# Kernel optimization log

Measured on AMD Instinct MI355X. Metric: run time of the kernel, lower is better.

Reference implementation:

```python
import jax, jax.numpy as jnp
import numpy as np

N_NODES = 100000
N_GRAPHS = 64
EPS = 1e-5


def _sage_conv(x, src, dst, Wl, bl, Wr):
    # mean-aggregate neighbor messages (src -> dst), then lin_l(agg) + lin_r(x)
    n = x.shape[0]
    deg = jax.ops.segment_sum(jnp.ones_like(dst, dtype=x.dtype), dst, num_segments=n)
    agg = jax.ops.segment_sum(x[src], dst, num_segments=n)  # [N, d]
    agg = agg / jnp.maximum(deg, 1.0)[:, None]
    return agg @ Wl + bl + x @ Wr


def _bn_relu(x, gamma, beta):
    mu = jnp.mean(x, axis=0)
    var = jnp.var(x, axis=0)
    return jax.nn.relu((x - mu) * jax.lax.rsqrt(var + EPS) * gamma + beta)


def setup_inputs() -> dict:
    key = jax.random.key(0)
    ks = jax.random.split(key, 16)
    E = 1600000
    x = jax.random.normal(ks[0], (N_NODES, 2), dtype=jnp.float32)
    edge_index = jax.random.randint(ks[1], (2, E), 0, N_NODES, dtype=jnp.int64)
    batch = jnp.sort(jax.random.randint(ks[2], (N_NODES,), 0, N_GRAPHS, dtype=jnp.int64))

    def lin(k, din, dout):
        s = 1.0 / np.sqrt(din)
        return jax.random.uniform(k, (din, dout), jnp.float32, -s, s)

    d = {"x": x, "edge_index": edge_index, "batch": batch}
    dims = [(2, 32), (32, 64), (64, 128)]
    for i, (din, dout) in enumerate(dims, 1):
        k1, k2 = jax.random.split(ks[2 + i])
        d[f"Wl{i}"] = lin(k1, din, dout)
        d[f"bl{i}"] = jnp.zeros((dout,), jnp.float32)
        d[f"Wr{i}"] = lin(k2, din, dout)
        d[f"g{i}"] = jnp.ones((dout,), jnp.float32)
        d[f"be{i}"] = jnp.zeros((dout,), jnp.float32)
    d["Wf1"] = lin(ks[10], 128, 64)
    d["bf1"] = jnp.zeros((64,), jnp.float32)
    d["Wf2"] = lin(ks[11], 64, 1)
    d["bf2"] = jnp.zeros((1,), jnp.float32)
    return d


def reference(x, edge_index, batch,
              Wl1, bl1, Wr1, g1, be1,
              Wl2, bl2, Wr2, g2, be2,
              Wl3, bl3, Wr3, g3, be3,
              Wf1, bf1, Wf2, bf2):
    src, dst = edge_index[0], edge_index[1]
    h = _bn_relu(_sage_conv(x, src, dst, Wl1, bl1, Wr1), g1, be1)
    h = _bn_relu(_sage_conv(h, src, dst, Wl2, bl2, Wr2), g2, be2)
    h = _bn_relu(_sage_conv(h, src, dst, Wl3, bl3, Wr3), g3, be3)
    # global mean pool over graphs
    cnt = jax.ops.segment_sum(jnp.ones_like(batch, dtype=h.dtype), batch, num_segments=N_GRAPHS)
    pooled = jax.ops.segment_sum(h, batch, num_segments=N_GRAPHS) / jnp.maximum(cnt, 1.0)[:, None]
    out = jax.nn.relu(pooled @ Wf1 + bf1)
    # dropout is identity in eval mode
    return out @ Wf2 + bf2
```

## Files before the change

kernel.cpp:

```cpp
#include <hip/hip_runtime.h>
#include <hip/hip_fp16.h>

#define N_NODES 100000
#define N_GRAPHS 64
#define BN_EPS 1e-5

#define NBF 391
#define PT1 4096
#define CAPF 4608

typedef _Float16 f16x8 __attribute__((ext_vector_type(8)));
typedef float f32x4 __attribute__((ext_vector_type(4)));

union F16x8u {
    f16x8 v;
    __half2 h2[4];
    uint4 u;
};

__device__ __forceinline__ float bfly64(float v) {
#pragma unroll
    for (int m = 1; m < 64; m <<= 1) v += __shfl_xor(v, m, 64);
    return v;
}

__device__ __forceinline__ unsigned pack_h2(float a, float b) {
    __half2 h = __floats2half2_rn(a, b);
    unsigned w;
    __builtin_memcpy(&w, &h, 4);
    return w;
}

__device__ __forceinline__ float2 unpack_h2(unsigned w) {
    __half2 h;
    __builtin_memcpy(&h, &w, 4);
    return __half22float2(h);
}

__global__ __launch_bounds__(256)
void pack_w(const float* __restrict__ Wl2, const float* __restrict__ Wr2,
            const float* __restrict__ Wl3, const float* __restrict__ Wr3,
            __half* __restrict__ pk, int* __restrict__ fcur,
            double* __restrict__ zero_region) {
    int tid = threadIdx.x;
    if (blockIdx.x == 0) {
        for (int t = tid; t < NBF; t += 256) fcur[t] = t * CAPF;
    } else if (blockIdx.x <= 4) {
        for (int i = (blockIdx.x - 1) * 256 + tid; i < 8960; i += 1024)
            zero_region[i] = 0.0;
    }
    int e = blockIdx.x * 256 + tid;
    const float* W; int le, DOUT, NCB, base, SZ;
    if (e < 2048)       { W = Wl2; le = e;         DOUT = 64;  NCB = 4; base = 0;     SZ = 2048; }
    else if (e < 4096)  { W = Wr2; le = e - 2048;  DOUT = 64;  NCB = 4; base = 4096;  SZ = 2048; }
    else if (e < 12288) { W = Wl3; le = e - 4096;  DOUT = 128; NCB = 8; base = 8192;  SZ = 8192; }
    else                { W = Wr3; le = e - 12288; DOUT = 128; NCB = 8; base = 24576; SZ = 8192; }
    int i = le & 7;
    int lane = (le >> 3) & 63;
    int cbkb = le >> 9;
    int cb = cbkb % NCB;
    int kb = cbkb / NCB;
    int k = kb * 32 + ((lane >> 4) << 3) + i;
    int col = cb * 16 + (lane & 15);
    float w = W[k * DOUT + col];
    __half h = __float2half(w);
    float lo = w - __half2float(h);
    pk[base + le] = h;
    pk[base + SZ + le] = __float2half(lo);
}


__global__ __launch_bounds__(256)
void part1(const int* __restrict__ dst, const int* __restrict__ src,
           int* __restrict__ fcur, int* __restrict__ qpk, int E) {
    __shared__ int ld[PT1];
    __shared__ unsigned short lb[PT1];
    __shared__ int hist[NBF], lbase[NBF], gbase[NBF];
    __shared__ int pairs[256];
    long long t0 = (long long)blockIdx.x * PT1;
    int n = (int)min((long long)PT1, (long long)E - t0);
    int tid = threadIdx.x;
    for (int i = tid; i < NBF; i += 256) hist[i] = 0;
    __syncthreads();
    int p[PT1 / 256], c[PT1 / 256];
#pragma unroll
    for (int k = 0; k < PT1 / 256; ++k) {
        int li = k * 256 + tid;
        if (li < n) {
            int d = __builtin_nontemporal_load(dst + t0 + li);
            int s = __builtin_nontemporal_load(src + t0 + li);
            c[k] = d >> 8;
            p[k] = ((d & 255) << 17) | s;
            atomicAdd(&hist[c[k]], 1);
        }
    }
    __syncthreads();
    int h0 = (2 * tid < NBF) ? hist[2 * tid] : 0;
    int h1 = (2 * tid + 1 < NBF) ? hist[2 * tid + 1] : 0;
    pairs[tid] = h0 + h1;
    __syncthreads();
    for (int st = 1; st < 256; st <<= 1) {
        int v = (tid >= st) ? pairs[tid - st] : 0;
        __syncthreads();
        pairs[tid] += v;
        __syncthreads();
    }
    int pe = tid ? pairs[tid - 1] : 0;
    if (2 * tid < NBF) lbase[2 * tid] = pe;
    if (2 * tid + 1 < NBF) lbase[2 * tid + 1] = pe + h0;
    __syncthreads();
    for (int b = tid; b < NBF; b += 256)
        gbase[b] = atomicAdd(&fcur[b], hist[b]);
    __syncthreads();
    for (int i = tid; i < NBF; i += 256) hist[i] = 0;
    __syncthreads();
#pragma unroll
    for (int k = 0; k < PT1 / 256; ++k) {
        int li = k * 256 + tid;
        if (li < n) {
            int pos = lbase[c[k]] + atomicAdd(&hist[c[k]], 1);
            ld[pos] = p[k]; lb[pos] = (unsigned short)c[k];
        }
    }
    __syncthreads();
    for (int i = tid; i < n; i += 256) {
        int bb = lb[i];
        int g = gbase[bb] + (i - lbase[bb]);
        qpk[g] = ld[i];
    }
}

__global__ __launch_bounds__(256)
void fill_final(const int* __restrict__ qpk, const int* __restrict__ fcur,
                int* __restrict__ offs, int* __restrict__ oend,
                int* __restrict__ nbr, int N) {
    __shared__ int cnt[256], cbase[256], cur[256];
    __shared__ int lout[CAPF];
    int b = blockIdx.x;
    int nlo = b << 8;
    int nn = min(256, N - nlo);
    int ebeg = b * CAPF;
    int ne = fcur[b] - ebeg;
    int tid = threadIdx.x;
    cnt[tid] = 0; cur[tid] = 0;
    __syncthreads();
    for (int i = tid; i < ne; i += 256)
        atomicAdd(&cnt[(qpk[ebeg + i] >> 17) & 255], 1);
    __syncthreads();
    cbase[tid] = cnt[tid];
    __syncthreads();
    for (int st = 1; st < 256; st <<= 1) {
        int v = (tid >= st) ? cbase[tid - st] : 0;
        __syncthreads();
        cbase[tid] += v;
        __syncthreads();
    }
    if (tid < nn) {
        offs[nlo + tid] = ebeg + (tid ? cbase[tid - 1] : 0);
        oend[nlo + tid] = ebeg + cbase[tid];
    }
    __syncthreads();
    for (int i = tid; i < ne; i += 256) {
        int p = qpk[ebeg + i];
        int ln = (p >> 17) & 255;
        int pos = (ln ? cbase[ln - 1] : 0) + atomicAdd(&cur[ln], 1);
        lout[pos] = p & 0x1FFFF;
    }
    __syncthreads();
    for (int i = tid; i < ne; i += 256)
        nbr[ebeg + i] = lout[i];
}

__global__ __launch_bounds__(256)
void layer1_fused(const float2* __restrict__ x2,
                  const int* __restrict__ offs, const int* __restrict__ oend,
                  const int* __restrict__ nbr,
                  const float* __restrict__ Wl, const float* __restrict__ bl,
                  const float* __restrict__ Wr,
                  __half* __restrict__ hout16,
                  double* __restrict__ sums, int N) {
    __shared__ float sAr[64];
    int tid = threadIdx.x;
    if (tid < 64) sAr[tid] = 0.f;
    __syncthreads();
    int n = blockIdx.x * 256 + tid;
    bool valid = (n < N);
    int beg = 0, end = 0;
    if (valid) { beg = offs[n]; end = oend[n]; }
    float ax0 = 0.f, ay0 = 0.f, ax1 = 0.f, ay1 = 0.f;
    int j = beg;
    for (; j + 16 <= end; j += 16) {
        int s[16];
#pragma unroll
        for (int u = 0; u < 16; ++u) s[u] = __builtin_nontemporal_load(nbr + j + u);
        float2 v[16];
#pragma unroll
        for (int u = 0; u < 16; ++u) v[u] = x2[s[u]];
#pragma unroll
        for (int u = 0; u < 16; ++u) {
            if (u & 1) { ax1 += v[u].x; ay1 += v[u].y; }
            else       { ax0 += v[u].x; ay0 += v[u].y; }
        }
    }
    for (; j + 4 <= end; j += 4) {
        int s[4];
#pragma unroll
        for (int u = 0; u < 4; ++u) s[u] = __builtin_nontemporal_load(nbr + j + u);
        float2 v[4];
#pragma unroll
        for (int u = 0; u < 4; ++u) v[u] = x2[s[u]];
        ax0 += v[0].x; ay0 += v[0].y;
        ax1 += v[1].x; ay1 += v[1].y;
        ax0 += v[2].x; ay0 += v[2].y;
        ax1 += v[3].x; ay1 += v[3].y;
    }
    for (; j < end; ++j) {
        float2 v = x2[nbr[j]];
        ax0 += v.x; ay0 += v.y;
    }
    float invd = 1.0f / fmaxf((float)(end - beg), 1.0f);
    float a0 = (ax0 + ax1) * invd, a1 = (ay0 + ay1) * invd;
    float x0 = 0.f, x1 = 0.f;
    if (valid) {
        float2 xv = x2[n];
        x0 = xv.x; x1 = xv.y;
    }
    float acc[32];
#pragma unroll
    for (int jj = 0; jj < 32; ++jj)
        acc[jj] = bl[jj] + a0 * Wl[jj] + a1 * Wl[32 + jj] + x0 * Wr[jj] + x1 * Wr[32 + jj];
    if (valid) {
        unsigned w[16];
#pragma unroll
        for (int p = 0; p < 16; ++p) w[p] = pack_h2(acc[2*p], acc[2*p+1]);
        uint4* q = (uint4*)(hout16 + (size_t)n * 32);
        q[0] = make_uint4(w[0], w[1], w[2], w[3]);
        q[1] = make_uint4(w[4], w[5], w[6], w[7]);
        q[2] = make_uint4(w[8], w[9], w[10], w[11]);
        q[3] = make_uint4(w[12], w[13], w[14], w[15]);
    }
    int lane = tid & 63;
#pragma unroll
    for (int jj = 0; jj < 32; ++jj) {
        float v = valid ? acc[jj] : 0.f;
        float s = bfly64(v);
        float q = bfly64(v * v);
        if (lane == jj) atomicAdd(&sAr[jj], s);
        if (lane == 32 + jj) atomicAdd(&sAr[32 + jj], q);
    }
    __syncthreads();
    if (tid < 64) atomicAdd(&sums[tid], (double)sAr[tid]);
}

template<int F>
__global__ __launch_bounds__(256)
void bn_apply(const uint4* __restrict__ h, const double* __restrict__ sums,
              const float* __restrict__ gamma, const float* __restrict__ beta,
              uint4* __restrict__ out, int N) {
    __shared__ __align__(16) float lsc[F], lsf[F];
    int tid = threadIdx.x;
    if (tid < F) {
        double mu = sums[tid] / (double)N_NODES;
        double var = sums[F + tid] / (double)N_NODES - mu * mu;
        if (var < 0.0) var = 0.0;
        double sc = (double)gamma[tid] / sqrt(var + BN_EPS);
        lsc[tid] = (float)sc;
        lsf[tid] = (float)((double)beta[tid] - mu * sc);
    }
    __syncthreads();
    constexpr int FV = F / 8;
    int total = N * FV;
    for (int i = blockIdx.x * 256 + tid; i < total; i += gridDim.x * 256) {
        uint4 v = h[i];
        int c4 = (i & (FV - 1)) * 2;
        float4 sca = ((const float4*)lsc)[c4];
        float4 scb = ((const float4*)lsc)[c4 + 1];
        float4 sfa = ((const float4*)lsf)[c4];
        float4 sfb = ((const float4*)lsf)[c4 + 1];
        float2 f0 = unpack_h2(v.x), f1 = unpack_h2(v.y);
        float2 f2 = unpack_h2(v.z), f3 = unpack_h2(v.w);
        uint4 o;
        o.x = pack_h2(fmaxf(f0.x * sca.x + sfa.x, 0.f), fmaxf(f0.y * sca.y + sfa.y, 0.f));
        o.y = pack_h2(fmaxf(f1.x * sca.z + sfa.z, 0.f), fmaxf(f1.y * sca.w + sfa.w, 0.f));
        o.z = pack_h2(fmaxf(f2.x * scb.x + sfb.x, 0.f), fmaxf(f2.y * scb.y + sfb.y, 0.f));
        o.w = pack_h2(fmaxf(f3.x * scb.z + sfb.z, 0.f), fmaxf(f3.y * scb.w + sfb.w, 0.f));
        out[i] = o;
    }
}

__device__ __forceinline__ void accum8_h16(float* acc, uint4 v) {
    float2 f0 = unpack_h2(v.x), f1 = unpack_h2(v.y);
    float2 f2 = unpack_h2(v.z), f3 = unpack_h2(v.w);
    acc[0] += f0.x; acc[1] += f0.y; acc[2] += f1.x; acc[3] += f1.y;
    acc[4] += f2.x; acc[5] += f2.y; acc[6] += f3.x; acc[7] += f3.y;
}

template<int F>
__global__ __launch_bounds__(256)
void agg_sum(const uint4* __restrict__ xb, const int* __restrict__ offs,
             const int* __restrict__ oend, const int* __restrict__ nbr,
             uint4* __restrict__ aggh, int N) {
    constexpr int FV = F / 8;
    constexpr int NPB = 256 / FV;
    int n = blockIdx.x * NPB + threadIdx.y;
    if (n >= N) return;
    int f = threadIdx.x;
    int beg = offs[n], end = oend[n];
    float a0[8], a1[8];
#pragma unroll
    for (int q = 0; q < 8; ++q) { a0[q] = 0.f; a1[q] = 0.f; }
    int j = beg;
    for (; j + 16 <= end; j += 16) {
        int s[16];
#pragma unroll
        for (int u = 0; u < 16; ++u) s[u] = __builtin_nontemporal_load(nbr + j + u);
        uint4 v[16];
#pragma unroll
        for (int u = 0; u < 16; ++u) v[u] = xb[s[u] * FV + f];
#pragma unroll
        for (int u = 0; u < 16; ++u)
            accum8_h16((u & 1) ? a1 : a0, v[u]);
    }
    if (j + 8 <= end) {
        int s[8];
#pragma unroll
        for (int u = 0; u < 8; ++u) s[u] = __builtin_nontemporal_load(nbr + j + u);
        uint4 v[8];
#pragma unroll
        for (int u = 0; u < 8; ++u) v[u] = xb[s[u] * FV + f];
#pragma unroll
        for (int u = 0; u < 8; ++u)
            accum8_h16((u & 1) ? a1 : a0, v[u]);
        j += 8;
    }
    if (j + 4 <= end) {
        int s[4];
#pragma unroll
        for (int u = 0; u < 4; ++u) s[u] = __builtin_nontemporal_load(nbr + j + u);
        uint4 v[4];
#pragma unroll
        for (int u = 0; u < 4; ++u) v[u] = xb[s[u] * FV + f];
#pragma unroll
        for (int u = 0; u < 4; ++u)
            accum8_h16((u & 1) ? a1 : a0, v[u]);
        j += 4;
    }
    for (; j < end; ++j) {
        uint4 v = xb[__builtin_nontemporal_load(nbr + j) * FV + f];
        accum8_h16(a0, v);
    }
    float invd = 1.0f / fmaxf((float)(end - beg), 1.0f);
    uint4 o;
    o.x = pack_h2((a0[0] + a1[0]) * invd, (a0[1] + a1[1]) * invd);
    o.y = pack_h2((a0[2] + a1[2]) * invd, (a0[3] + a1[3]) * invd);
    o.z = pack_h2((a0[4] + a1[4]) * invd, (a0[5] + a1[5]) * invd);
    o.w = pack_h2((a0[6] + a1[6]) * invd, (a0[7] + a1[7]) * invd);
    aggh[n * FV + f] = o;
}

template<int DIN, int DOUT>
__global__ __launch_bounds__(256)
void linear_mfma(const __half* __restrict__ bnx16, const __half* __restrict__ agg16,
                 const __half* __restrict__ wlhi, const __half* __restrict__ wllo,
                 const __half* __restrict__ wrhi, const __half* __restrict__ wrlo,
                 const float* __restrict__ bl,
                 __half* __restrict__ hout16, float* __restrict__ partial, int N) {
    constexpr int KB = DIN / 32;
    constexpr int NCB = DOUT / 16;
    constexpr int MREP = 2;
    constexpr int MB = 4 * MREP * 16;
    __shared__ float blkS[DOUT], blkQ[DOUT];
    int tid = threadIdx.x;
    for (int i = tid; i < DOUT; i += 256) { blkS[i] = 0.f; blkQ[i] = 0.f; }
    __syncthreads();
    int n0 = blockIdx.x * MB;

    int wave = tid >> 6;
    int lane = tid & 63;
    int rlane = lane & 15;
    int kg = lane >> 4;
    int rbase = n0 + wave * (MREP * 16);

    f16x8 aA[MREP][KB], aX[MREP][KB];
#pragma unroll
    for (int m = 0; m < MREP; ++m) {
        int row = rbase + m * 16 + rlane;
        int rowc = min(row, N - 1);
#pragma unroll
        for (int kb = 0; kb < KB; ++kb) {
            int c0 = kb * 32 + kg * 8;
            F16x8u ta, tx;
            ta.u = *(const uint4*)(agg16 + (size_t)rowc * DIN + c0);
            tx.u = *(const uint4*)(bnx16 + (size_t)rowc * DIN + c0);
            aA[m][kb] = ta.v;
            aX[m][kb] = tx.v;
        }
    }

    f32x4 acc[MREP][NCB];
#pragma unroll
    for (int cb = 0; cb < NCB; ++cb) {
        float bv = bl[cb * 16 + rlane];
#pragma unroll
        for (int m = 0; m < MREP; ++m)
            acc[m][cb] = {bv, bv, bv, bv};
    }

#pragma unroll
    for (int cb = 0; cb < NCB; ++cb) {
#pragma unroll
        for (int kb = 0; kb < KB; ++kb) {
            size_t fo = ((size_t)(kb * NCB + cb) * 64 + lane) * 8;
            f16x8 blh = *(const f16x8*)(wlhi + fo);
            f16x8 bll = *(const f16x8*)(wllo + fo);
            f16x8 brh = *(const f16x8*)(wrhi + fo);
            f16x8 brl = *(const f16x8*)(wrlo + fo);
#pragma unroll
            for (int m = 0; m < MREP; ++m) {
                acc[m][cb] = __builtin_amdgcn_mfma_f32_16x16x32_f16(aA[m][kb], blh, acc[m][cb], 0, 0, 0);
                acc[m][cb] = __builtin_amdgcn_mfma_f32_16x16x32_f16(aA[m][kb], bll, acc[m][cb], 0, 0, 0);
                acc[m][cb] = __builtin_amdgcn_mfma_f32_16x16x32_f16(aX[m][kb], brh, acc[m][cb], 0, 0, 0);
                acc[m][cb] = __builtin_amdgcn_mfma_f32_16x16x32_f16(aX[m][kb], brl, acc[m][cb], 0, 0, 0);
            }
        }
    }

#pragma unroll
    for (int m = 0; m < MREP; ++m) {
        int rowb = rbase + m * 16 + kg * 4;
#pragma unroll
        for (int r = 0; r < 4; ++r) {
            int node = rowb + r;
            if (node < N) {
#pragma unroll
                for (int cb = 0; cb < NCB; ++cb)
                    hout16[(size_t)node * DOUT + cb * 16 + rlane] = __float2half(acc[m][cb][r]);
            }
        }
    }

#pragma unroll
    for (int cb = 0; cb < NCB; ++cb) {
        float s = 0.f, q = 0.f;
#pragma unroll
        for (int m = 0; m < MREP; ++m) {
            int rowb = rbase + m * 16 + kg * 4;
#pragma unroll
            for (int r = 0; r < 4; ++r) {
                if (rowb + r < N) {
                    float v = acc[m][cb][r];
                    s += v; q += v * v;
                }
            }
        }
        s += __shfl_xor(s, 16, 64); s += __shfl_xor(s, 32, 64);
        q += __shfl_xor(q, 16, 64); q += __shfl_xor(q, 32, 64);
        if (kg == 0) {
            atomicAdd(&blkS[cb * 16 + rlane], s);
            atomicAdd(&blkQ[cb * 16 + rlane], q);
        }
    }
    __syncthreads();
    float* po = partial + (size_t)blockIdx.x * (2 * DOUT);
    for (int i = tid; i < DOUT; i += 256) {
        po[i] = blkS[i];
        po[DOUT + i] = blkQ[i];
    }
}

template<int F>
__global__ __launch_bounds__(256)
void stats_finalize2(const float* __restrict__ partial, double* __restrict__ sums, int P) {
    __shared__ double sh[256];
    int i = blockIdx.x;
    int t = threadIdx.x;
    double a = 0.0;
    for (int k = t; k < P; k += 256)
        a += (double)partial[(size_t)k * (2 * F) + i];
    sh[t] = a;
    __syncthreads();
    for (int st = 128; st > 0; st >>= 1) {
        if (t < st) sh[t] += sh[t + st];
        __syncthreads();
    }
    if (t == 0) sums[i] = sh[0];
}

__global__ void pool_partial(const __half* __restrict__ h, const int* __restrict__ batch,
                             const double* __restrict__ sums,
                             const float* __restrict__ gamma, const float* __restrict__ beta,
                             double* __restrict__ pooled_d, int N) {
    __shared__ float lsc[128], lsf[128];
    const int CH = 64;
    int f = threadIdx.x;
    {
        double mu = sums[f] / (double)N_NODES;
        double var = sums[128 + f] / (double)N_NODES - mu * mu;
        if (var < 0.0) var = 0.0;
        double sc = (double)gamma[f] / sqrt(var + BN_EPS);
        lsc[f] = (float)sc;
        lsf[f] = (float)((double)beta[f] - mu * sc);
    }
    __syncthreads();
    int n0 = blockIdx.x * CH;
    if (n0 >= N) return;
    int n1 = min(n0 + CH, N);
    float sc = lsc[f], sf = lsf[f];
    int g = batch[n0];
    float acc = 0.f;
    for (int n = n0; n < n1; ++n) {
        int bg = batch[n];
        if (bg != g) {
            atomicAdd(&pooled_d[g * 128 + f], (double)acc);
            acc = 0.f;
            g = bg;
        }
        float v = __half2float(h[(long long)n * 128 + f]);
        acc += fmaxf(v * sc + sf, 0.f);
    }
    atomicAdd(&pooled_d[g * 128 + f], (double)acc);
}

__global__ void mlp_fused(const double* __restrict__ pooled_d, const int* __restrict__ batch,
                          const float* __restrict__ Wf1, const float* __restrict__ bf1,
                          const float* __restrict__ Wf2, const float* __restrict__ bf2,
                          float* __restrict__ out, int N) {
    __shared__ float sp[128];
    int g = blockIdx.x;
    int t = threadIdx.x;
    int lo = 0, hi = N;
    while (lo < hi) { int m = (lo + hi) >> 1; if (batch[m] < g) lo = m + 1; else hi = m; }
    int start = lo;
    hi = N;
    while (lo < hi) { int m = (lo + hi) >> 1; if (batch[m] < g + 1) lo = m + 1; else hi = m; }
    int cnt = lo - start;
    sp[t] = (float)(pooled_d[g * 128 + t] / (double)max(cnt, 1));
    __syncthreads();
    if (t < 64) {
        float hacc = bf1[t];
#pragma unroll 8
        for (int k = 0; k < 128; ++k) hacc += sp[k] * Wf1[k * 64 + t];
        hacc = fmaxf(hacc, 0.f) * Wf2[t];
        for (int o = 32; o > 0; o >>= 1) hacc += __shfl_down(hacc, o);
        if (t == 0) out[g] = hacc + bf2[0];
    }
}

extern "C" void kernel_launch(void* const* d_in, const int* in_sizes, int n_in,
                              void* d_out, int out_size, void* d_ws, size_t ws_size,
                              hipStream_t stream) {
    const float* x     = (const float*)d_in[0];
    const int*   ei    = (const int*)d_in[1];
    const int*   batch = (const int*)d_in[2];
    const float *Wl1=(const float*)d_in[3],  *bl1=(const float*)d_in[4],  *Wr1=(const float*)d_in[5];
    const float *g1 =(const float*)d_in[6],  *be1=(const float*)d_in[7];
    const float *Wl2=(const float*)d_in[8],  *bl2=(const float*)d_in[9],  *Wr2=(const float*)d_in[10];
    const float *g2 =(const float*)d_in[11], *be2=(const float*)d_in[12];
    const float *Wl3=(const float*)d_in[13], *bl3=(const float*)d_in[14], *Wr3=(const float*)d_in[15];
    const float *g3 =(const float*)d_in[16], *be3=(const float*)d_in[17];
    const float *Wf1=(const float*)d_in[18], *bf1=(const float*)d_in[19];
    const float *Wf2=(const float*)d_in[20], *bf2=(const float*)d_in[21];

    const int N = N_NODES;
    const int E = in_sizes[1] / 2;
    const int* src = ei;
    const int* dst = ei + E;

    char* ws = (char*)d_ws;
    size_t off = 0;
    auto salloc = [&](size_t bytes) {
        void* p = ws + off;
        off += (bytes + 255) & ~(size_t)255;
        return p;
    };
    double* sums    = (double*)salloc(768 * 8);
    double* pooledd = (double*)salloc((size_t)N_GRAPHS * 128 * 8);
    int*    offs    = (int*)   salloc((size_t)N * 4);
    int*    oend    = (int*)   salloc((size_t)N * 4);
    int*    fcur    = (int*)   salloc((NBF + 1) * 4);
    int*    nbr     = (int*)   salloc((size_t)NBF * CAPF * 4);
    float*  partial = (float*) salloc((size_t)1024 * 256 * 4);
    __half* pk      = (__half*)salloc((size_t)40960 * 2);
    __half* h1h     = (__half*)salloc((size_t)(N + 256) * 32 * 2);
    __half* b1h     = (__half*)salloc((size_t)(N + 256) * 32 * 2);
    __half* h2h     = (__half*)salloc((size_t)(N + 256) * 64 * 2);
    __half* b2h     = (__half*)salloc((size_t)(N + 256) * 64 * 2);
    __half* h3h     = (__half*)salloc((size_t)(N + 256) * 128 * 2);
    __half* aggh    = (__half*)salloc((size_t)(N + 256) * 64 * 2);
    (void)ws_size;

    double* sums1 = sums, *sums2 = sums + 256, *sums3 = sums + 512;
    int* qpk = (int*)aggh;

    const __half *pwl2h = pk,         *pwl2l = pk + 2048;
    const __half *pwr2h = pk + 4096,  *pwr2l = pk + 6144;
    const __half *pwl3h = pk + 8192,  *pwl3l = pk + 16384;
    const __half *pwr3h = pk + 24576, *pwr3l = pk + 32768;

    pack_w<<<80, 256, 0, stream>>>(Wl2, Wr2, Wl3, Wr3, pk, fcur, sums);

    part1<<<(E + PT1 - 1) / PT1, 256, 0, stream>>>(dst, src, fcur, qpk, E);
    fill_final<<<NBF, 256, 0, stream>>>(qpk, fcur, offs, oend, nbr, N);

    const int NL = (N + 255) / 256;
    const int NBLK = (N + 127) / 128;

    layer1_fused<<<NL, 256, 0, stream>>>((const float2*)x, offs, oend, nbr,
                                          Wl1, bl1, Wr1, h1h, sums1, N);

    bn_apply<32><<<512, 256, 0, stream>>>((const uint4*)h1h, sums1, g1, be1, (uint4*)b1h, N);
    agg_sum<32><<<(N + 63) / 64, dim3(4, 64), 0, stream>>>(
        (const uint4*)b1h, offs, oend, nbr, (uint4*)aggh, N);
    linear_mfma<32, 64><<<NBLK, 256, 0, stream>>>(
        b1h, (const __half*)aggh, pwl2h, pwl2l, pwr2h, pwr2l, bl2, h2h, partial, N);
    stats_finalize2<64><<<128, 256, 0, stream>>>(partial, sums2, NBLK);

    bn_apply<64><<<512, 256, 0, stream>>>((const uint4*)h2h, sums2, g2, be2, (uint4*)b2h, N);
    agg_sum<64><<<(N + 31) / 32, dim3(8, 32), 0, stream>>>(
        (const uint4*)b2h, offs, oend, nbr, (uint4*)aggh, N);
    linear_mfma<64, 128><<<NBLK, 256, 0, stream>>>(
        b2h, (const __half*)aggh, pwl3h, pwl3l, pwr3h, pwr3l, bl3, h3h, partial, N);
    stats_finalize2<128><<<256, 256, 0, stream>>>(partial, sums3, NBLK);

    pool_partial<<<(N + 63) / 64, 128, 0, stream>>>(h3h, batch, sums3, g3, be3, pooledd, N);
    mlp_fused<<<N_GRAPHS, 128, 0, stream>>>(pooledd, batch, Wf1, bf1, Wf2, bf2, (float*)d_out, N);
}
```

Measured before the change: 304.9 us.

## Fuse BatchNorm+ReLU into neighbor aggregation and linear kernels, drop bn_apply

Removes the standalone bn_apply passes that wrote normalized copies of layer 1 and layer 2 activations. The scale/shift is now recomputed per block and applied on the fly, both on each gathered neighbor row in the aggregation kernel and on the self features in the MFMA linear kernel. This saves two kernel launches and a full read-and-write of the activation tensors. In exchange the aggregation does extra FMA/max work per gathered edge (about 16 edges per node), and the self path rounds an extra time to half precision.

```diff
diff --git a/kernel.cpp b/kernel.cpp
--- a/kernel.cpp
+++ b/kernel.cpp
@@ -252,13 +252,30 @@
     if (tid < 64) atomicAdd(&sums[tid], (double)sAr[tid]);
 }
 
+__device__ __forceinline__ void accum8_bn(float* acc, uint4 v,
+                                          const float* sc, const float* sf) {
+    float2 f0 = unpack_h2(v.x), f1 = unpack_h2(v.y);
+    float2 f2 = unpack_h2(v.z), f3 = unpack_h2(v.w);
+    acc[0] += fmaxf(f0.x * sc[0] + sf[0], 0.f);
+    acc[1] += fmaxf(f0.y * sc[1] + sf[1], 0.f);
+    acc[2] += fmaxf(f1.x * sc[2] + sf[2], 0.f);
+    acc[3] += fmaxf(f1.y * sc[3] + sf[3], 0.f);
+    acc[4] += fmaxf(f2.x * sc[4] + sf[4], 0.f);
+    acc[5] += fmaxf(f2.y * sc[5] + sf[5], 0.f);
+    acc[6] += fmaxf(f3.x * sc[6] + sf[6], 0.f);
+    acc[7] += fmaxf(f3.y * sc[7] + sf[7], 0.f);
+}
+
 template<int F>
 __global__ __launch_bounds__(256)
-void bn_apply(const uint4* __restrict__ h, const double* __restrict__ sums,
-              const float* __restrict__ gamma, const float* __restrict__ beta,
-              uint4* __restrict__ out, int N) {
-    __shared__ __align__(16) float lsc[F], lsf[F];
-    int tid = threadIdx.x;
+void agg_bn(const uint4* __restrict__ xh, const int* __restrict__ offs,
+            const int* __restrict__ oend, const int* __restrict__ nbr,
+            const double* __restrict__ sums, const float* __restrict__ gamma,
+            const float* __restrict__ beta, uint4* __restrict__ aggh, int N) {
+    constexpr int FV = F / 8;
+    constexpr int NPB = 256 / FV;
+    __shared__ float lsc[F], lsf[F];
+    int tid = threadIdx.y * FV + threadIdx.x;
     if (tid < F) {
         double mu = sums[tid] / (double)N_NODES;
         double var = sums[F + tid] / (double)N_NODES - mu * mu;
@@ -268,43 +285,12 @@
         lsf[tid] = (float)((double)beta[tid] - mu * sc);
     }
     __syncthreads();
-    constexpr int FV = F / 8;
-    int total = N * FV;
-    for (int i = blockIdx.x * 256 + tid; i < total; i += gridDim.x * 256) {
-        uint4 v = h[i];
-        int c4 = (i & (FV - 1)) * 2;
-        float4 sca = ((const float4*)lsc)[c4];
-        float4 scb = ((const float4*)lsc)[c4 + 1];
-        float4 sfa = ((const float4*)lsf)[c4];
-        float4 sfb = ((const float4*)lsf)[c4 + 1];
-        float2 f0 = unpack_h2(v.x), f1 = unpack_h2(v.y);
-        float2 f2 = unpack_h2(v.z), f3 = unpack_h2(v.w);
-        uint4 o;
-        o.x = pack_h2(fmaxf(f0.x * sca.x + sfa.x, 0.f), fmaxf(f0.y * sca.y + sfa.y, 0.f));
-        o.y = pack_h2(fmaxf(f1.x * sca.z + sfa.z, 0.f), fmaxf(f1.y * sca.w + sfa.w, 0.f));
-        o.z = pack_h2(fmaxf(f2.x * scb.x + sfb.x, 0.f), fmaxf(f2.y * scb.y + sfb.y, 0.f));
-        o.w = pack_h2(fmaxf(f3.x * scb.z + sfb.z, 0.f), fmaxf(f3.y * scb.w + sfb.w, 0.f));
-        out[i] = o;
-    }
-}
-
-__device__ __forceinline__ void accum8_h16(float* acc, uint4 v) {
-    float2 f0 = unpack_h2(v.x), f1 = unpack_h2(v.y);
-    float2 f2 = unpack_h2(v.z), f3 = unpack_h2(v.w);
-    acc[0] += f0.x; acc[1] += f0.y; acc[2] += f1.x; acc[3] += f1.y;
-    acc[4] += f2.x; acc[5] += f2.y; acc[6] += f3.x; acc[7] += f3.y;
-}
-
-template<int F>
-__global__ __launch_bounds__(256)
-void agg_sum(const uint4* __restrict__ xb, const int* __restrict__ offs,
-             const int* __restrict__ oend, const int* __restrict__ nbr,
-             uint4* __restrict__ aggh, int N) {
-    constexpr int FV = F / 8;
-    constexpr int NPB = 256 / FV;
     int n = blockIdx.x * NPB + threadIdx.y;
     if (n >= N) return;
     int f = threadIdx.x;
+    float sc[8], sf[8];
+#pragma unroll
+    for (int q = 0; q < 8; ++q) { sc[q] = lsc[f * 8 + q]; sf[q] = lsf[f * 8 + q]; }
     int beg = offs[n], end = oend[n];
     float a0[8], a1[8];
 #pragma unroll
@@ -316,10 +302,10 @@
         for (int u = 0; u < 16; ++u) s[u] = __builtin_nontemporal_load(nbr + j + u);
         uint4 v[16];
 #pragma unroll
-        for (int u = 0; u < 16; ++u) v[u] = xb[s[u] * FV + f];
+        for (int u = 0; u < 16; ++u) v[u] = xh[s[u] * FV + f];
 #pragma unroll
         for (int u = 0; u < 16; ++u)
-            accum8_h16((u & 1) ? a1 : a0, v[u]);
+            accum8_bn((u & 1) ? a1 : a0, v[u], sc, sf);
     }
     if (j + 8 <= end) {
         int s[8];
@@ -327,10 +313,10 @@
         for (int u = 0; u < 8; ++u) s[u] = __builtin_nontemporal_load(nbr + j + u);
         uint4 v[8];
 #pragma unroll
-        for (int u = 0; u < 8; ++u) v[u] = xb[s[u] * FV + f];
+        for (int u = 0; u < 8; ++u) v[u] = xh[s[u] * FV + f];
 #pragma unroll
         for (int u = 0; u < 8; ++u)
-            accum8_h16((u & 1) ? a1 : a0, v[u]);
+            accum8_bn((u & 1) ? a1 : a0, v[u], sc, sf);
         j += 8;
     }
     if (j + 4 <= end) {
@@ -339,15 +325,15 @@
         for (int u = 0; u < 4; ++u) s[u] = __builtin_nontemporal_load(nbr + j + u);
         uint4 v[4];
 #pragma unroll
-        for (int u = 0; u < 4; ++u) v[u] = xb[s[u] * FV + f];
+        for (int u = 0; u < 4; ++u) v[u] = xh[s[u] * FV + f];
 #pragma unroll
         for (int u = 0; u < 4; ++u)
-            accum8_h16((u & 1) ? a1 : a0, v[u]);
+            accum8_bn((u & 1) ? a1 : a0, v[u], sc, sf);
         j += 4;
     }
     for (; j < end; ++j) {
-        uint4 v = xb[__builtin_nontemporal_load(nbr + j) * FV + f];
-        accum8_h16(a0, v);
+        uint4 v = xh[__builtin_nontemporal_load(nbr + j) * FV + f];
+        accum8_bn(a0, v, sc, sf);
     }
     float invd = 1.0f / fmaxf((float)(end - beg), 1.0f);
     uint4 o;
@@ -360,17 +346,28 @@
 
 template<int DIN, int DOUT>
 __global__ __launch_bounds__(256)
-void linear_mfma(const __half* __restrict__ bnx16, const __half* __restrict__ agg16,
+void linear_mfma(const __half* __restrict__ xh, const __half* __restrict__ agg16,
                  const __half* __restrict__ wlhi, const __half* __restrict__ wllo,
                  const __half* __restrict__ wrhi, const __half* __restrict__ wrlo,
                  const float* __restrict__ bl,
+                 const double* __restrict__ sumsIn,
+                 const float* __restrict__ gIn, const float* __restrict__ beIn,
                  __half* __restrict__ hout16, float* __restrict__ partial, int N) {
     constexpr int KB = DIN / 32;
     constexpr int NCB = DOUT / 16;
     constexpr int MREP = 2;
     constexpr int MB = 4 * MREP * 16;
     __shared__ float blkS[DOUT], blkQ[DOUT];
+    __shared__ __align__(16) float lscIn[DIN], lsfIn[DIN];
     int tid = threadIdx.x;
+    if (tid < DIN) {
+        double mu = sumsIn[tid] / (double)N_NODES;
+        double var = sumsIn[DIN + tid] / (double)N_NODES - mu * mu;
+        if (var < 0.0) var = 0.0;
+        double sc = (double)gIn[tid] / sqrt(var + BN_EPS);
+        lscIn[tid] = (float)sc;
+        lsfIn[tid] = (float)((double)beIn[tid] - mu * sc);
+    }
     for (int i = tid; i < DOUT; i += 256) { blkS[i] = 0.f; blkQ[i] = 0.f; }
     __syncthreads();
     int n0 = blockIdx.x * MB;
@@ -391,7 +388,23 @@
             int c0 = kb * 32 + kg * 8;
             F16x8u ta, tx;
             ta.u = *(const uint4*)(agg16 + (size_t)rowc * DIN + c0);
-            tx.u = *(const uint4*)(bnx16 + (size_t)rowc * DIN + c0);
+            tx.u = *(const uint4*)(xh + (size_t)rowc * DIN + c0);
+            float4 sca = ((const float4*)lscIn)[c0 >> 2];
+            float4 scb = ((const float4*)lscIn)[(c0 >> 2) + 1];
+            float4 sfa = ((const float4*)lsfIn)[c0 >> 2];
+            float4 sfb = ((const float4*)lsfIn)[(c0 >> 2) + 1];
+            float2 f0 = __half22float2(tx.h2[0]);
+            float2 f1 = __half22float2(tx.h2[1]);
+            float2 f2 = __half22float2(tx.h2[2]);
+            float2 f3 = __half22float2(tx.h2[3]);
+            tx.h2[0] = __floats2half2_rn(fmaxf(f0.x * sca.x + sfa.x, 0.f),
+                                         fmaxf(f0.y * sca.y + sfa.y, 0.f));
+            tx.h2[1] = __floats2half2_rn(fmaxf(f1.x * sca.z + sfa.z, 0.f),
+                                         fmaxf(f1.y * sca.w + sfa.w, 0.f));
+            tx.h2[2] = __floats2half2_rn(fmaxf(f2.x * scb.x + sfb.x, 0.f),
+                                         fmaxf(f2.y * scb.y + sfb.y, 0.f));
+            tx.h2[3] = __floats2half2_rn(fmaxf(f3.x * scb.z + sfb.z, 0.f),
+                                         fmaxf(f3.y * scb.w + sfb.w, 0.f));
             aA[m][kb] = ta.v;
             aX[m][kb] = tx.v;
         }
@@ -582,9 +595,7 @@
     float*  partial = (float*) salloc((size_t)1024 * 256 * 4);
     __half* pk      = (__half*)salloc((size_t)40960 * 2);
     __half* h1h     = (__half*)salloc((size_t)(N + 256) * 32 * 2);
-    __half* b1h     = (__half*)salloc((size_t)(N + 256) * 32 * 2);
     __half* h2h     = (__half*)salloc((size_t)(N + 256) * 64 * 2);
-    __half* b2h     = (__half*)salloc((size_t)(N + 256) * 64 * 2);
     __half* h3h     = (__half*)salloc((size_t)(N + 256) * 128 * 2);
     __half* aggh    = (__half*)salloc((size_t)(N + 256) * 64 * 2);
     (void)ws_size;
@@ -608,18 +619,18 @@
     layer1_fused<<<NL, 256, 0, stream>>>((const float2*)x, offs, oend, nbr,
                                           Wl1, bl1, Wr1, h1h, sums1, N);
 
-    bn_apply<32><<<512, 256, 0, stream>>>((const uint4*)h1h, sums1, g1, be1, (uint4*)b1h, N);
-    agg_sum<32><<<(N + 63) / 64, dim3(4, 64), 0, stream>>>(
-        (const uint4*)b1h, offs, oend, nbr, (uint4*)aggh, N);
+    agg_bn<32><<<(N + 63) / 64, dim3(4, 64), 0, stream>>>(
+        (const uint4*)h1h, offs, oend, nbr, sums1, g1, be1, (uint4*)aggh, N);
     linear_mfma<32, 64><<<NBLK, 256, 0, stream>>>(
-        b1h, (const __half*)aggh, pwl2h, pwl2l, pwr2h, pwr2l, bl2, h2h, partial, N);
+        h1h, (const __half*)aggh, pwl2h, pwl2l, pwr2h, pwr2l, bl2,
+        sums1, g1, be1, h2h, partial, N);
     stats_finalize2<64><<<128, 256, 0, stream>>>(partial, sums2, NBLK);
 
-    bn_apply<64><<<512, 256, 0, stream>>>((const uint4*)h2h, sums2, g2, be2, (uint4*)b2h, N);
-    agg_sum<64><<<(N + 31) / 32, dim3(8, 32), 0, stream>>>(
-        (const uint4*)b2h, offs, oend, nbr, (uint4*)aggh, N);
+    agg_bn<64><<<(N + 31) / 32, dim3(8, 32), 0, stream>>>(
+        (const uint4*)h2h, offs, oend, nbr, sums2, g2, be2, (uint4*)aggh, N);
     linear_mfma<64, 128><<<NBLK, 256, 0, stream>>>(
-        b2h, (const __half*)aggh, pwl3h, pwl3l, pwr3h, pwr3l, bl3, h3h, partial, N);
+        h2h, (const __half*)aggh, pwl3h, pwl3l, pwr3h, pwr3l, bl3,
+        sums2, g2, be2, h3h, partial, N);
     stats_finalize2<128><<<256, 256, 0, stream>>>(partial, sums3, NBLK);
 
     pool_partial<<<(N + 63) / 64, 128, 0, stream>>>(h3h, batch, sums3, g3, be3, pooledd, N);
```

Measured after the change: 310.5 us. No clear change (+1.8%).

## Store BN outputs and aggregates feature-slice-major to shrink gather working set

Applied to the files above, without the earlier changes.

BN-apply now writes its output transposed into feature slices of 8 halves (slice-major, node-minor) through a shared-memory tile. Aggregation runs one slice per block, so each gather touches only a 1.6 MB slice that fits better in cache. The MFMA linear kernel reads its A operands from the slice layout. In exchange the transpose adds shared-memory staging and barriers, the neighbor list is re-read once per slice, and the linear loads become strided across slices.

```diff
diff --git a/kernel.cpp b/kernel.cpp
--- a/kernel.cpp
+++ b/kernel.cpp
@@ -6,6 +6,7 @@
 #define BN_EPS 1e-5
 
 #define NBF 391
+#define NP  (NBF * 256)
 #define PT1 4096
 #define CAPF 4608
 
@@ -254,10 +255,13 @@
 
 template<int F>
 __global__ __launch_bounds__(256)
-void bn_apply(const uint4* __restrict__ h, const double* __restrict__ sums,
-              const float* __restrict__ gamma, const float* __restrict__ beta,
-              uint4* __restrict__ out, int N) {
+void bn_apply_t(const uint4* __restrict__ h, const double* __restrict__ sums,
+                const float* __restrict__ gamma, const float* __restrict__ beta,
+                uint4* __restrict__ out_t, int N) {
+    constexpr int FV = F / 8;
+    constexpr int NT = 256 / FV;
     __shared__ __align__(16) float lsc[F], lsf[F];
+    __shared__ uint4 tile[FV * (NT + 1)];
     int tid = threadIdx.x;
     if (tid < F) {
         double mu = sums[tid] / (double)N_NODES;
@@ -268,23 +272,33 @@
         lsf[tid] = (float)((double)beta[tid] - mu * sc);
     }
     __syncthreads();
-    constexpr int FV = F / 8;
-    int total = N * FV;
-    for (int i = blockIdx.x * 256 + tid; i < total; i += gridDim.x * 256) {
-        uint4 v = h[i];
-        int c4 = (i & (FV - 1)) * 2;
-        float4 sca = ((const float4*)lsc)[c4];
-        float4 scb = ((const float4*)lsc)[c4 + 1];
-        float4 sfa = ((const float4*)lsf)[c4];
-        float4 sfb = ((const float4*)lsf)[c4 + 1];
-        float2 f0 = unpack_h2(v.x), f1 = unpack_h2(v.y);
-        float2 f2 = unpack_h2(v.z), f3 = unpack_h2(v.w);
-        uint4 o;
-        o.x = pack_h2(fmaxf(f0.x * sca.x + sfa.x, 0.f), fmaxf(f0.y * sca.y + sfa.y, 0.f));
-        o.y = pack_h2(fmaxf(f1.x * sca.z + sfa.z, 0.f), fmaxf(f1.y * sca.w + sfa.w, 0.f));
-        o.z = pack_h2(fmaxf(f2.x * scb.x + sfb.x, 0.f), fmaxf(f2.y * scb.y + sfb.y, 0.f));
-        o.w = pack_h2(fmaxf(f3.x * scb.z + sfb.z, 0.f), fmaxf(f3.y * scb.w + sfb.w, 0.f));
-        out[i] = o;
+    int f = tid % FV;
+    int nl = tid / FV;
+    float4 sca = ((const float4*)lsc)[f * 2];
+    float4 scb = ((const float4*)lsc)[f * 2 + 1];
+    float4 sfa = ((const float4*)lsf)[f * 2];
+    float4 sfb = ((const float4*)lsf)[f * 2 + 1];
+    int fo = tid / NT;
+    int no = tid % NT;
+    int ntiles = (N + NT - 1) / NT;
+    for (int t = blockIdx.x; t < ntiles; t += gridDim.x) {
+        int n0 = t * NT;
+        int n = n0 + nl;
+        uint4 o = make_uint4(0u, 0u, 0u, 0u);
+        if (n < N) {
+            uint4 v = h[(size_t)n * FV + f];
+            float2 f0 = unpack_h2(v.x), f1 = unpack_h2(v.y);
+            float2 f2 = unpack_h2(v.z), f3 = unpack_h2(v.w);
+            o.x = pack_h2(fmaxf(f0.x * sca.x + sfa.x, 0.f), fmaxf(f0.y * sca.y + sfa.y, 0.f));
+            o.y = pack_h2(fmaxf(f1.x * sca.z + sfa.z, 0.f), fmaxf(f1.y * sca.w + sfa.w, 0.f));
+            o.z = pack_h2(fmaxf(f2.x * scb.x + sfb.x, 0.f), fmaxf(f2.y * scb.y + sfb.y, 0.f));
+            o.w = pack_h2(fmaxf(f3.x * scb.z + sfb.z, 0.f), fmaxf(f3.y * scb.w + sfb.w, 0.f));
+        }
+        tile[f * (NT + 1) + nl] = o;
+        __syncthreads();
+        int nn = n0 + no;
+        if (nn < N) out_t[(size_t)fo * NP + nn] = tile[fo * (NT + 1) + no];
+        __syncthreads();
     }
 }
 
@@ -297,14 +311,14 @@
 
 template<int F>
 __global__ __launch_bounds__(256)
-void agg_sum(const uint4* __restrict__ xb, const int* __restrict__ offs,
-             const int* __restrict__ oend, const int* __restrict__ nbr,
-             uint4* __restrict__ aggh, int N) {
+void agg_slice(const uint4* __restrict__ bt, const int* __restrict__ offs,
+               const int* __restrict__ oend, const int* __restrict__ nbr,
+               uint4* __restrict__ aggt, int N) {
     constexpr int FV = F / 8;
-    constexpr int NPB = 256 / FV;
-    int n = blockIdx.x * NPB + threadIdx.y;
+    int f = blockIdx.x % FV;
+    int n = (blockIdx.x / FV) * 256 + threadIdx.x;
     if (n >= N) return;
-    int f = threadIdx.x;
+    const uint4* __restrict__ xb = bt + (size_t)f * NP;
     int beg = offs[n], end = oend[n];
     float a0[8], a1[8];
 #pragma unroll
@@ -316,7 +330,7 @@
         for (int u = 0; u < 16; ++u) s[u] = __builtin_nontemporal_load(nbr + j + u);
         uint4 v[16];
 #pragma unroll
-        for (int u = 0; u < 16; ++u) v[u] = xb[s[u] * FV + f];
+        for (int u = 0; u < 16; ++u) v[u] = xb[s[u]];
 #pragma unroll
         for (int u = 0; u < 16; ++u)
             accum8_h16((u & 1) ? a1 : a0, v[u]);
@@ -327,7 +341,7 @@
         for (int u = 0; u < 8; ++u) s[u] = __builtin_nontemporal_load(nbr + j + u);
         uint4 v[8];
 #pragma unroll
-        for (int u = 0; u < 8; ++u) v[u] = xb[s[u] * FV + f];
+        for (int u = 0; u < 8; ++u) v[u] = xb[s[u]];
 #pragma unroll
         for (int u = 0; u < 8; ++u)
             accum8_h16((u & 1) ? a1 : a0, v[u]);
@@ -339,28 +353,26 @@
         for (int u = 0; u < 4; ++u) s[u] = __builtin_nontemporal_load(nbr + j + u);
         uint4 v[4];
 #pragma unroll
-        for (int u = 0; u < 4; ++u) v[u] = xb[s[u] * FV + f];
+        for (int u = 0; u < 4; ++u) v[u] = xb[s[u]];
 #pragma unroll
         for (int u = 0; u < 4; ++u)
             accum8_h16((u & 1) ? a1 : a0, v[u]);
         j += 4;
     }
-    for (; j < end; ++j) {
-        uint4 v = xb[__builtin_nontemporal_load(nbr + j) * FV + f];
-        accum8_h16(a0, v);
-    }
+    for (; j < end; ++j)
+        accum8_h16(a0, xb[__builtin_nontemporal_load(nbr + j)]);
     float invd = 1.0f / fmaxf((float)(end - beg), 1.0f);
     uint4 o;
     o.x = pack_h2((a0[0] + a1[0]) * invd, (a0[1] + a1[1]) * invd);
     o.y = pack_h2((a0[2] + a1[2]) * invd, (a0[3] + a1[3]) * invd);
     o.z = pack_h2((a0[4] + a1[4]) * invd, (a0[5] + a1[5]) * invd);
     o.w = pack_h2((a0[6] + a1[6]) * invd, (a0[7] + a1[7]) * invd);
-    aggh[n * FV + f] = o;
+    aggt[(size_t)f * NP + n] = o;
 }
 
 template<int DIN, int DOUT>
 __global__ __launch_bounds__(256)
-void linear_mfma(const __half* __restrict__ bnx16, const __half* __restrict__ agg16,
+void linear_mfma(const uint4* __restrict__ bt, const uint4* __restrict__ aggt,
                  const __half* __restrict__ wlhi, const __half* __restrict__ wllo,
                  const __half* __restrict__ wrhi, const __half* __restrict__ wrlo,
                  const float* __restrict__ bl,
@@ -388,10 +400,10 @@
         int rowc = min(row, N - 1);
 #pragma unroll
         for (int kb = 0; kb < KB; ++kb) {
-            int c0 = kb * 32 + kg * 8;
+            int sl = kb * 4 + kg;
             F16x8u ta, tx;
-            ta.u = *(const uint4*)(agg16 + (size_t)rowc * DIN + c0);
-            tx.u = *(const uint4*)(bnx16 + (size_t)rowc * DIN + c0);
+            ta.u = aggt[(size_t)sl * NP + rowc];
+            tx.u = bt[(size_t)sl * NP + rowc];
             aA[m][kb] = ta.v;
             aX[m][kb] = tx.v;
         }
@@ -582,15 +594,15 @@
     float*  partial = (float*) salloc((size_t)1024 * 256 * 4);
     __half* pk      = (__half*)salloc((size_t)40960 * 2);
     __half* h1h     = (__half*)salloc((size_t)(N + 256) * 32 * 2);
-    __half* b1h     = (__half*)salloc((size_t)(N + 256) * 32 * 2);
+    uint4*  b1t     = (uint4*) salloc((size_t)4 * NP * 16);
     __half* h2h     = (__half*)salloc((size_t)(N + 256) * 64 * 2);
-    __half* b2h     = (__half*)salloc((size_t)(N + 256) * 64 * 2);
+    uint4*  b2t     = (uint4*) salloc((size_t)8 * NP * 16);
     __half* h3h     = (__half*)salloc((size_t)(N + 256) * 128 * 2);
-    __half* aggh    = (__half*)salloc((size_t)(N + 256) * 64 * 2);
+    uint4*  aggt    = (uint4*) salloc((size_t)8 * NP * 16);
     (void)ws_size;
 
     double* sums1 = sums, *sums2 = sums + 256, *sums3 = sums + 512;
-    int* qpk = (int*)aggh;
+    int* qpk = (int*)aggt;
 
     const __half *pwl2h = pk,         *pwl2l = pk + 2048;
     const __half *pwr2h = pk + 4096,  *pwr2l = pk + 6144;
@@ -608,18 +620,16 @@
     layer1_fused<<<NL, 256, 0, stream>>>((const float2*)x, offs, oend, nbr,
                                           Wl1, bl1, Wr1, h1h, sums1, N);
 
-    bn_apply<32><<<512, 256, 0, stream>>>((const uint4*)h1h, sums1, g1, be1, (uint4*)b1h, N);
-    agg_sum<32><<<(N + 63) / 64, dim3(4, 64), 0, stream>>>(
-        (const uint4*)b1h, offs, oend, nbr, (uint4*)aggh, N);
+    bn_apply_t<32><<<512, 256, 0, stream>>>((const uint4*)h1h, sums1, g1, be1, b1t, N);
+    agg_slice<32><<<4 * NBF, 256, 0, stream>>>(b1t, offs, oend, nbr, aggt, N);
     linear_mfma<32, 64><<<NBLK, 256, 0, stream>>>(
-        b1h, (const __half*)aggh, pwl2h, pwl2l, pwr2h, pwr2l, bl2, h2h, partial, N);
+        b1t, aggt, pwl2h, pwl2l, pwr2h, pwr2l, bl2, h2h, partial, N);
     stats_finalize2<64><<<128, 256, 0, stream>>>(partial, sums2, NBLK);
 
-    bn_apply<64><<<512, 256, 0, stream>>>((const uint4*)h2h, sums2, g2, be2, (uint4*)b2h, N);
-    agg_sum<64><<<(N + 31) / 32, dim3(8, 32), 0, stream>>>(
-        (const uint4*)b2h, offs, oend, nbr, (uint4*)aggh, N);
+    bn_apply_t<64><<<512, 256, 0, stream>>>((const uint4*)h2h, sums2, g2, be2, b2t, N);
+    agg_slice<64><<<8 * NBF, 256, 0, stream>>>(b2t, offs, oend, nbr, aggt, N);
     linear_mfma<64, 128><<<NBLK, 256, 0, stream>>>(
-        b2h, (const __half*)aggh, pwl3h, pwl3l, pwr3h, pwr3l, bl3, h3h, partial, N);
+        b2t, aggt, pwl3h, pwl3l, pwr3h, pwr3l, bl3, h3h, partial, N);
     stats_finalize2<128><<<256, 256, 0, stream>>>(partial, sums3, NBLK);
 
     pool_partial<<<(N + 63) / 64, 128, 0, stream>>>(h3h, batch, sums3, g3, be3, pooledd, N);
```

Result: slower. 403.4 us (+32.3%).
